# Performance work log

Measured on AMD Instinct MI355X. Metric: run time of the kernel, lower is better.

The kernel has to match this reference:

```python
import jax, jax.numpy as jnp
import numpy as np

B, D, H = 4096, 256, 1024
TRACE_STEPS = 10
T_FINAL = 1.0


def setup_inputs() -> dict:
    key = jax.random.key(0)
    k0, k1, k2 = jax.random.split(key, 3)
    s1 = 1.0 / np.sqrt(D + 1)
    s2 = 1.0 / np.sqrt(H)
    return {
        "x": jax.random.normal(k0, (B, D), dtype=jnp.float32),
        "W1": jax.random.uniform(k1, (D + 1, H), jnp.float32, -s1, s1),
        "b1": jnp.zeros((H,), jnp.float32),
        "W2": jax.random.uniform(k2, (H, D), jnp.float32, -s2, s2),
        "b2": jnp.zeros((D,), jnp.float32),
    }


def _odefun(params, t, z):
    # FFJORD vector field: tanh MLP on [z, t]. z: [B, D] -> [B, D]
    W1, b1, W2, b2 = params
    tcol = jnp.full((z.shape[0], 1), t, dtype=z.dtype)
    h = jnp.tanh(jnp.concatenate([z, tcol], axis=-1) @ W1 + b1)
    return h @ W2 + b2


def _rademacher(key, shape, dtype):
    # randint(0,2)*2-1, matching the torch probe construction
    return jax.random.randint(key, shape, 0, 2).astype(dtype) * 2.0 - 1.0


def _aug_dynamics(params, t, state, e):
    # state: [B, D+1] = [z | logp]; e: [TRACE_STEPS, B, D] Rademacher probes.
    # torch computes etf = grad((f*e).sum(), z) = e^T J, div = (e^T J)*e summed.
    # e^T J e == e . (J e), so forward-mode jvp gives identical math.
    z = state[:, :-1]
    f = lambda zz: _odefun(params, t, zz)

    def probe(ei):
        f_z, Je = jax.jvp(f, (z,), (ei,))
        return f_z, jnp.sum(Je * ei, axis=-1)  # [B]

    f_z, divs = jax.vmap(probe)(e)
    f_z = f_z[0]                       # primal identical across probes
    div_est = jnp.mean(divs, axis=0)   # average of trace_steps estimates
    return jnp.concatenate([f_z, -div_est[:, None]], axis=-1)


def reference(x, W1, b1, W2, b2):
    params = (W1, b1, W2, b2)
    Bx = x.shape[0]
    ekey = jax.random.key(42)
    probes = lambda i: _rademacher(jax.random.fold_in(ekey, i), (TRACE_STEPS, Bx, D), x.dtype)

    # initial augmented state: [z, logp=0]
    y0 = jnp.concatenate([x, jnp.zeros((Bx, 1), x.dtype)], axis=-1)

    # t_grid = [0, T] with 2 points -> fixed-grid rk4 takes ONE RK4 step of size T
    h = T_FINAL
    g = lambda t, y, i: _aug_dynamics(params, t, y, probes(i))
    k1 = g(0.0, y0, 0)
    k2 = g(0.5 * h, y0 + 0.5 * h * k1, 1)
    k3 = g(0.5 * h, y0 + 0.5 * h * k2, 2)
    k4 = g(h, y0 + h * k3, 3)
    y1 = y0 + (h / 6.0) * (k1 + 2.0 * k2 + 2.0 * k3 + k4)

    # module returns the full trajectory `output`: [len(t_grid), B, D+1]
    return jnp.stack([y0, y1], axis=0)
```

## Files before the change

### kernel.cpp

```cpp
#include <hip/hip_runtime.h>
#include <stdint.h>

#define BATCH 4096
#define DIMD  256
#define DIMH  1024
#define NEEL  10485760
#define NSLOT 1310720

typedef __attribute__((ext_vector_type(8))) short short8;
typedef __attribute__((ext_vector_type(4))) float float4v;

struct Keys4 { uint32_t a[4]; uint32_t b[4]; };

__host__ __device__ static inline uint32_t rotl32(uint32_t v, int r) {
#ifdef __HIP_DEVICE_COMPILE__
    return __builtin_amdgcn_alignbit(v, v, 32 - r);
#else
    return (v << r) | (v >> (32 - r));
#endif
}

__host__ __device__ static inline void tf2x32(uint32_t k0, uint32_t k1,
                                              uint32_t c0, uint32_t c1,
                                              uint32_t& o0, uint32_t& o1) {
    uint32_t ks0 = k0, ks1 = k1, ks2 = k0 ^ k1 ^ 0x1BD11BDAu;
    uint32_t x0 = c0 + ks0, x1 = c1 + ks1;
#define TF_R4(a, b, c, d)                                   \
    x0 += x1; x1 = rotl32(x1, a); x1 ^= x0;                 \
    x0 += x1; x1 = rotl32(x1, b); x1 ^= x0;                 \
    x0 += x1; x1 = rotl32(x1, c); x1 ^= x0;                 \
    x0 += x1; x1 = rotl32(x1, d); x1 ^= x0;
    TF_R4(13, 15, 26, 6)  x0 += ks1; x1 += ks2 + 1u;
    TF_R4(17, 29, 16, 24) x0 += ks2; x1 += ks0 + 2u;
    TF_R4(13, 15, 26, 6)  x0 += ks0; x1 += ks1 + 3u;
    TF_R4(17, 29, 16, 24) x0 += ks1; x1 += ks2 + 4u;
    TF_R4(13, 15, 26, 6)  x0 += ks2; x1 += ks0 + 5u;
#undef TF_R4
    o0 = x0; o1 = x1;
}

__device__ static inline short f2bf(float f) {
    uint32_t u = __float_as_uint(f);
    uint32_t r = (u + 0x7FFFu + ((u >> 16) & 1u)) >> 16;
    return (short)r;
}

__device__ static inline void egen_slot(short* __restrict__ EF, uint32_t q,
                                        uint32_t k0, uint32_t k1) {
    const uint32_t lane = q & 63u;
    const uint32_t ks   = (q >> 6) & 7u;
    const uint32_t T    = (q >> 9) & 255u;
    const uint32_t probe = q >> 17;
    const uint32_t b = T * 16u + (lane & 15u);
    const uint32_t d0 = ks * 32u + (lane >> 4) * 8u;
    const uint32_t jbase = (probe * 4096u + b) * 256u + d0;
    short8 val;
#pragma unroll
    for (int jj = 0; jj < 8; ++jj) {
        uint32_t y0, y1;
        tf2x32(k0, k1, 0u, jbase + (uint32_t)jj, y0, y1);
        val[jj] = ((y0 ^ y1) & 1u) ? (short)0x3F80 : (short)0xBF80u;
    }
    *(short8*)&EF[(size_t)q * 8] = val;
}

__global__ __launch_bounds__(256) void k_prep(
    const float* __restrict__ x,  const float* __restrict__ W1,
    const float* __restrict__ W2, short* __restrict__ W1T,
    short* __restrict__ W2B, short* __restrict__ W2T,
    short* __restrict__ zb, float* __restrict__ dv,
    short* __restrict__ E0, uint32_t ek0, uint32_t ek1)
{
    const int idx = blockIdx.x * 256 + threadIdx.x;
    if (idx < 262144) {
        const int n = idx >> 8, d = idx & 255;
        W1T[idx] = f2bf(W1[d * DIMH + n]);
    } else if (idx < 524288) {
        const int i = idx - 262144;
        W2B[i] = f2bf(W2[i]);
    } else if (idx < 786432) {
        const int i = idx - 524288;
        const int d = i >> 10, k = i & 1023;
        W2T[i] = f2bf(W2[k * DIMD + d]);
    } else if (idx < 1835008) {
        const int i = idx - 786432;
        zb[i] = f2bf(x[i]);
    } else if (idx < 1851392) {
        dv[idx - 1835008] = 0.0f;
    } else {
        egen_slot(E0, (uint32_t)(idx - 1851392), ek0, ek1);
    }
}

__global__ __launch_bounds__(256) void k_pre_div(
    const short* __restrict__ Zb, const short* __restrict__ W1T,
    const short* __restrict__ W2B, const float* __restrict__ W1,
    const float* __restrict__ b1, float tval,
    const short* __restrict__ Ecur, short* __restrict__ h_bf,
    float* __restrict__ divacc,
    short* __restrict__ Enext, uint32_t nk0, uint32_t nk1, int do_egen)
{
    __shared__ short8 Es[4096];
    const int t = threadIdx.x;
    const int b0 = blockIdx.x * 64;
    const int nt = blockIdx.y;
    const int wave = t >> 6, lane = t & 63;
    const int col = lane & 15, kq = lane >> 4;
    const int n = nt * 64 + wave * 16 + col;

    short8 bufr[8], bvfr[8];
#pragma unroll
    for (int ks = 0; ks < 8; ++ks) {
        bufr[ks] = *(const short8*)&W1T[n * DIMD + ks * 32 + kq * 8];
        bvfr[ks] = *(const short8*)&W2B[n * DIMD + ks * 32 + kq * 8];
    }

    float sreg[4][4];
    const float add = tval * W1[DIMD * DIMH + n] + b1[n];
#pragma unroll
    for (int ms = 0; ms < 4; ++ms) {
        float4v acc = {0.f, 0.f, 0.f, 0.f};
#pragma unroll
        for (int ks = 0; ks < 8; ++ks) {
            short8 af = *(const short8*)&Zb[(b0 + ms * 16 + col) * DIMD + ks * 32 + kq * 8];
            acc = __builtin_amdgcn_mfma_f32_16x16x32_bf16(af, bufr[ks], acc, 0, 0, 0);
        }
#pragma unroll
        for (int r = 0; r < 4; ++r) {
            float hv = tanhf(acc[r] + add);
            h_bf[(b0 + ms * 16 + kq * 4 + r) * DIMH + n] = f2bf(hv);
            sreg[ms][r] = 1.0f - hv * hv;
        }
    }

    float rowacc[4][4];
#pragma unroll
    for (int a = 0; a < 4; ++a)
#pragma unroll
        for (int r = 0; r < 4; ++r) rowacc[a][r] = 0.0f;

    const uint32_t bflat = (uint32_t)(blockIdx.y * 64 + blockIdx.x);
    const uint32_t qbase = bflat * 256u + (uint32_t)t;

    const int Tb = b0 >> 4;

#pragma unroll 1
    for (int pp = 0; pp < 5; ++pp) {
        if (do_egen) {
            egen_slot(Enext, qbase + (uint32_t)pp * 262144u, nk0, nk1);
        }
        const short8* src0 = (const short8*)Ecur + (size_t)((2 * pp) * 256 + Tb) * 512;
        const short8* src1 = src0 + (size_t)256 * 512;
        __syncthreads();
#pragma unroll
        for (int k = 0; k < 8; ++k)
            Es[t + k * 256] = src0[t + k * 256];
#pragma unroll
        for (int k = 0; k < 8; ++k)
            Es[2048 + t + k * 256] = src1[t + k * 256];
        __syncthreads();

#pragma unroll
        for (int half = 0; half < 2; ++half) {
#pragma unroll
            for (int ms = 0; ms < 4; ++ms) {
                float4v u = {0.f, 0.f, 0.f, 0.f}, v = {0.f, 0.f, 0.f, 0.f};
#pragma unroll
                for (int ks = 0; ks < 8; ++ks) {
                    short8 af = Es[half * 2048 + ((ms * 8 + ks) << 6) + lane];
                    u = __builtin_amdgcn_mfma_f32_16x16x32_bf16(af, bufr[ks], u, 0, 0, 0);
                    v = __builtin_amdgcn_mfma_f32_16x16x32_bf16(af, bvfr[ks], v, 0, 0, 0);
                }
#pragma unroll
                for (int r = 0; r < 4; ++r)
                    rowacc[ms][r] += u[r] * sreg[ms][r] * v[r];
            }
        }
    }

#pragma unroll
    for (int ms = 0; ms < 4; ++ms) {
#pragma unroll
        for (int r = 0; r < 4; ++r) {
            float p = rowacc[ms][r];
            p += __shfl_xor(p, 1, 64);
            p += __shfl_xor(p, 2, 64);
            p += __shfl_xor(p, 4, 64);
            p += __shfl_xor(p, 8, 64);
            rowacc[ms][r] = p;
        }
    }
    if (col == 0) {
#pragma unroll
        for (int ms = 0; ms < 4; ++ms)
#pragma unroll
            for (int r = 0; r < 4; ++r)
                atomicAdd(&divacc[b0 + ms * 16 + kq * 4 + r], rowacc[ms][r] * 0.1f);
    }
}

__global__ __launch_bounds__(256) void k_fz2(
    const short* __restrict__ Hb, const short* __restrict__ W2T,
    const float* __restrict__ b2, const float* __restrict__ x,
    float* __restrict__ rksum, float cw, int first,
    float cnext, int write_zb, short* __restrict__ zb,
    int final_out, const float* __restrict__ dv, float* __restrict__ out)
{
    const int t = threadIdx.x;
    const int wave = t >> 6, lane = t & 63;
    const int col = lane & 15, kq = lane >> 4;
    const int m0 = blockIdx.x * 16;
    const int n0 = wave * 64;
    const int TOT = BATCH * (DIMD + 1);
    const float sixth = 1.0f / 6.0f;

    float4v acc[4];
#pragma unroll
    for (int ns = 0; ns < 4; ++ns) acc[ns] = (float4v){0.f, 0.f, 0.f, 0.f};

    const short* ap = &Hb[(m0 + col) * DIMH + kq * 8];
    short8 a_cur = *(const short8*)ap;
    short8 b_cur[4];
#pragma unroll
    for (int ns = 0; ns < 4; ++ns)
        b_cur[ns] = *(const short8*)&W2T[(n0 + ns * 16 + col) * DIMH + kq * 8];

    for (int ks = 0; ks < 31; ++ks) {
        short8 a_nxt = *(const short8*)&ap[(ks + 1) * 32];
        short8 b_nxt[4];
#pragma unroll
        for (int ns = 0; ns < 4; ++ns)
            b_nxt[ns] = *(const short8*)&W2T[(n0 + ns * 16 + col) * DIMH + (ks + 1) * 32 + kq * 8];
#pragma unroll
        for (int ns = 0; ns < 4; ++ns)
            acc[ns] = __builtin_amdgcn_mfma_f32_16x16x32_bf16(a_cur, b_cur[ns], acc[ns], 0, 0, 0);
        a_cur = a_nxt;
#pragma unroll
        for (int ns = 0; ns < 4; ++ns) b_cur[ns] = b_nxt[ns];
    }
#pragma unroll
    for (int ns = 0; ns < 4; ++ns)
        acc[ns] = __builtin_amdgcn_mfma_f32_16x16x32_bf16(a_cur, b_cur[ns], acc[ns], 0, 0, 0);

#pragma unroll
    for (int ns = 0; ns < 4; ++ns) {
        const int n = n0 + ns * 16 + col;
        const float bias = b2[n];
#pragma unroll
        for (int r = 0; r < 4; ++r) {
            const int m = m0 + kq * 4 + r;
            const int o = m * DIMD + n;
            const float val = acc[ns][r] + bias;
            if (final_out) {
                const float xv = x[o];
                out[m * (DIMD + 1) + n] = xv;
                out[TOT + m * (DIMD + 1) + n] =
                    xv + (rksum[o] + val) * sixth;
            } else {
                const float contrib = cw * val;
                rksum[o] = first ? contrib : (rksum[o] + contrib);
                if (write_zb)
                    zb[o] = f2bf(x[o] + cnext * val);
            }
        }
    }

    if (final_out && wave == 3 && col == 0) {
#pragma unroll
        for (int r = 0; r < 4; ++r) {
            const int m = m0 + kq * 4 + r;
            const float d1 = dv[m];
            const float d2 = dv[BATCH + m];
            const float d3 = dv[2 * BATCH + m];
            const float d4 = dv[3 * BATCH + m];
            out[m * (DIMD + 1) + DIMD] = 0.0f;
            out[TOT + m * (DIMD + 1) + DIMD] =
                -(d1 + 2.0f * d2 + 2.0f * d3 + d4) * sixth;
        }
    }
}

extern "C" void kernel_launch(void* const* d_in, const int* in_sizes, int n_in,
                              void* d_out, int out_size, void* d_ws, size_t ws_size,
                              hipStream_t stream) {
    const float* x  = (const float*)d_in[0];
    const float* W1 = (const float*)d_in[1];
    const float* b1 = (const float*)d_in[2];
    const float* W2 = (const float*)d_in[3];
    const float* b2 = (const float*)d_in[4];
    float* out = (float*)d_out;

    char* ws = (char*)d_ws;
    short* hb    = (short*)(ws);
    float* rksum = (float*)(ws + 8388608);
    short* zb    = (short*)(ws + 12582912);
    short* w1t   = (short*)(ws + 14680064);
    short* w2b   = (short*)(ws + 15204352);
    short* w2t   = (short*)(ws + 15728640);
    float* dv    = (float*)(ws + 16252928);
    short* e0    = (short*)(ws + 16318464);
    short* e1    = (short*)(ws + 37289984);

    Keys4 keys;
    for (uint32_t i = 0; i < 4; ++i) {
        uint32_t f0, f1, g0, g1;
        tf2x32(0u, 42u, 0u, i, f0, f1);
        tf2x32(f0, f1, 0u, 1u, g0, g1);
        keys.a[i] = g0;
        keys.b[i] = g1;
    }

    k_prep<<<12352, 256, 0, stream>>>(x, W1, W2, w1t, w2b, w2t, zb, dv,
                                      e0, keys.a[0], keys.b[0]);

    const float tvals[4] = {0.0f, 0.5f, 0.5f, 1.0f};
    const float cnext[4] = {0.5f, 0.5f, 1.0f, 0.0f};
    const float cw[4]    = {1.0f, 2.0f, 2.0f, 1.0f};
    for (int s = 0; s < 4; ++s) {
        const int last = (s == 3);
        short* ecur = (s & 1) ? e1 : e0;
        short* enxt = (s & 1) ? e0 : e1;
        k_pre_div<<<dim3(64, 16), 256, 0, stream>>>(
            zb, w1t, w2b, W1, b1, tvals[s], ecur,
            hb, dv + (size_t)s * BATCH,
            enxt, last ? 0u : keys.a[s + 1], last ? 0u : keys.b[s + 1],
            last ? 0 : 1);
        k_fz2<<<256, 256, 0, stream>>>(hb, w2t, b2, x, rksum,
                                       cw[s], (s == 0) ? 1 : 0,
                                       cnext[s], (s < 3) ? 1 : 0, zb,
                                       last ? 1 : 0, dv, out);
    }
}
```

Baseline: 482.6 us.

## Double-buffer probe tiles with async global-to-LDS loads and split output GEMM grid

```diff
diff --git a/kernel.cpp b/kernel.cpp
--- a/kernel.cpp
+++ b/kernel.cpp
@@ -43,6 +43,12 @@
     uint32_t u = __float_as_uint(f);
     uint32_t r = (u + 0x7FFFu + ((u >> 16) & 1u)) >> 16;
     return (short)r;
+}
+
+__device__ static inline void async_cp16(const void* gsrc, void* ldst) {
+    typedef __attribute__((address_space(1))) const unsigned int GU;
+    typedef __attribute__((address_space(3))) unsigned int LU;
+    __builtin_amdgcn_global_load_lds((GU*)gsrc, (LU*)ldst, 16, 0, 0);
 }
 
 __device__ static inline void egen_slot(short* __restrict__ EF, uint32_t q,
@@ -100,13 +106,29 @@
     float* __restrict__ divacc,
     short* __restrict__ Enext, uint32_t nk0, uint32_t nk1, int do_egen)
 {
-    __shared__ short8 Es[4096];
+    __shared__ short8 Es[2][2048];
     const int t = threadIdx.x;
     const int b0 = blockIdx.x * 64;
     const int nt = blockIdx.y;
     const int wave = t >> 6, lane = t & 63;
     const int col = lane & 15, kq = lane >> 4;
     const int n = nt * 64 + wave * 16 + col;
+    const int Tb = b0 >> 4;
+
+    const short8* Ebase = (const short8*)Ecur;
+    auto stage = [&](int p) {
+        const short8* src = Ebase + (size_t)(p * 256 + Tb) * 512 + wave * 64;
+        short8* dst = &Es[p & 1][wave * 64];
+#pragma unroll
+        for (int k = 0; k < 8; ++k)
+            async_cp16(src + k * 256 + lane, dst + k * 256);
+    };
+    stage(0);
+    stage(1);
+
+    const uint32_t bflat = (uint32_t)(blockIdx.y * 64 + blockIdx.x);
+    const uint32_t qbase = bflat * 256u + (uint32_t)t;
+    if (do_egen) egen_slot(Enext, qbase, nk0, nk1);
 
     short8 bufr[8], bvfr[8];
 #pragma unroll
@@ -139,43 +161,32 @@
 #pragma unroll
         for (int r = 0; r < 4; ++r) rowacc[a][r] = 0.0f;
 
-    const uint32_t bflat = (uint32_t)(blockIdx.y * 64 + blockIdx.x);
-    const uint32_t qbase = bflat * 256u + (uint32_t)t;
-
-    const int Tb = b0 >> 4;
-
 #pragma unroll 1
-    for (int pp = 0; pp < 5; ++pp) {
-        if (do_egen) {
-            egen_slot(Enext, qbase + (uint32_t)pp * 262144u, nk0, nk1);
-        }
-        const short8* src0 = (const short8*)Ecur + (size_t)((2 * pp) * 256 + Tb) * 512;
-        const short8* src1 = src0 + (size_t)256 * 512;
-        __syncthreads();
-#pragma unroll
-        for (int k = 0; k < 8; ++k)
-            Es[t + k * 256] = src0[t + k * 256];
-#pragma unroll
-        for (int k = 0; k < 8; ++k)
-            Es[2048 + t + k * 256] = src1[t + k * 256];
-        __syncthreads();
-
-#pragma unroll
-        for (int half = 0; half < 2; ++half) {
-#pragma unroll
-            for (int ms = 0; ms < 4; ++ms) {
-                float4v u = {0.f, 0.f, 0.f, 0.f}, v = {0.f, 0.f, 0.f, 0.f};
-#pragma unroll
-                for (int ks = 0; ks < 8; ++ks) {
-                    short8 af = Es[half * 2048 + ((ms * 8 + ks) << 6) + lane];
-                    u = __builtin_amdgcn_mfma_f32_16x16x32_bf16(af, bufr[ks], u, 0, 0, 0);
-                    v = __builtin_amdgcn_mfma_f32_16x16x32_bf16(af, bvfr[ks], v, 0, 0, 0);
-                }
-#pragma unroll
-                for (int r = 0; r < 4; ++r)
-                    rowacc[ms][r] += u[r] * sreg[ms][r] * v[r];
+    for (int pp = 0; pp < 10; ++pp) {
+        if (pp < 9) { asm volatile("s_waitcnt vmcnt(8)" ::: "memory"); }
+        else        { asm volatile("s_waitcnt vmcnt(0)" ::: "memory"); }
+        __builtin_amdgcn_s_barrier();
+
+        const short8* buf = (const short8*)Es[pp & 1];
+#pragma unroll
+        for (int ms = 0; ms < 4; ++ms) {
+            float4v u = {0.f, 0.f, 0.f, 0.f}, v = {0.f, 0.f, 0.f, 0.f};
+#pragma unroll
+            for (int ks = 0; ks < 8; ++ks) {
+                short8 af = buf[ms * 512 + ks * 64 + lane];
+                u = __builtin_amdgcn_mfma_f32_16x16x32_bf16(af, bufr[ks], u, 0, 0, 0);
+                v = __builtin_amdgcn_mfma_f32_16x16x32_bf16(af, bvfr[ks], v, 0, 0, 0);
             }
-        }
+#pragma unroll
+            for (int r = 0; r < 4; ++r)
+                rowacc[ms][r] += u[r] * sreg[ms][r] * v[r];
+        }
+
+        asm volatile("" ::: "memory");
+        __builtin_amdgcn_s_barrier();
+        if (pp < 8) stage(pp + 2);
+        if (do_egen && (pp & 1) == 0 && pp <= 6)
+            egen_slot(Enext, qbase + (uint32_t)(1 + (pp >> 1)) * 262144u, nk0, nk1);
     }
 
 #pragma unroll
@@ -210,51 +221,38 @@
     const int wave = t >> 6, lane = t & 63;
     const int col = lane & 15, kq = lane >> 4;
     const int m0 = blockIdx.x * 16;
-    const int n0 = wave * 64;
+    const int n0 = blockIdx.y * 64 + wave * 16;
     const int TOT = BATCH * (DIMD + 1);
     const float sixth = 1.0f / 6.0f;
 
-    float4v acc[4];
-#pragma unroll
-    for (int ns = 0; ns < 4; ++ns) acc[ns] = (float4v){0.f, 0.f, 0.f, 0.f};
+    float4v acc = {0.f, 0.f, 0.f, 0.f};
 
     const short* ap = &Hb[(m0 + col) * DIMH + kq * 8];
+    const short* bp = &W2T[(n0 + col) * DIMH + kq * 8];
     short8 a_cur = *(const short8*)ap;
-    short8 b_cur[4];
-#pragma unroll
-    for (int ns = 0; ns < 4; ++ns)
-        b_cur[ns] = *(const short8*)&W2T[(n0 + ns * 16 + col) * DIMH + kq * 8];
+    short8 b_cur = *(const short8*)bp;
 
     for (int ks = 0; ks < 31; ++ks) {
         short8 a_nxt = *(const short8*)&ap[(ks + 1) * 32];
-        short8 b_nxt[4];
-#pragma unroll
-        for (int ns = 0; ns < 4; ++ns)
-            b_nxt[ns] = *(const short8*)&W2T[(n0 + ns * 16 + col) * DIMH + (ks + 1) * 32 + kq * 8];
-#pragma unroll
-        for (int ns = 0; ns < 4; ++ns)
-            acc[ns] = __builtin_amdgcn_mfma_f32_16x16x32_bf16(a_cur, b_cur[ns], acc[ns], 0, 0, 0);
+        short8 b_nxt = *(const short8*)&bp[(ks + 1) * 32];
+        acc = __builtin_amdgcn_mfma_f32_16x16x32_bf16(a_cur, b_cur, acc, 0, 0, 0);
         a_cur = a_nxt;
-#pragma unroll
-        for (int ns = 0; ns < 4; ++ns) b_cur[ns] = b_nxt[ns];
-    }
-#pragma unroll
-    for (int ns = 0; ns < 4; ++ns)
-        acc[ns] = __builtin_amdgcn_mfma_f32_16x16x32_bf16(a_cur, b_cur[ns], acc[ns], 0, 0, 0);
-
-#pragma unroll
-    for (int ns = 0; ns < 4; ++ns) {
-        const int n = n0 + ns * 16 + col;
-        const float bias = b2[n];
+        b_cur = b_nxt;
+    }
+    acc = __builtin_amdgcn_mfma_f32_16x16x32_bf16(a_cur, b_cur, acc, 0, 0, 0);
+
+    {
+        const int nn = n0 + col;
+        const float bias = b2[nn];
 #pragma unroll
         for (int r = 0; r < 4; ++r) {
             const int m = m0 + kq * 4 + r;
-            const int o = m * DIMD + n;
-            const float val = acc[ns][r] + bias;
+            const int o = m * DIMD + nn;
+            const float val = acc[r] + bias;
             if (final_out) {
                 const float xv = x[o];
-                out[m * (DIMD + 1) + n] = xv;
-                out[TOT + m * (DIMD + 1) + n] =
+                out[m * (DIMD + 1) + nn] = xv;
+                out[TOT + m * (DIMD + 1) + nn] =
                     xv + (rksum[o] + val) * sixth;
             } else {
                 const float contrib = cw * val;
@@ -265,7 +263,7 @@
         }
     }
 
-    if (final_out && wave == 3 && col == 0) {
+    if (final_out && blockIdx.y == 0 && wave == 0 && col == 0) {
 #pragma unroll
         for (int r = 0; r < 4; ++r) {
             const int m = m0 + kq * 4 + r;
@@ -325,9 +323,9 @@
             hb, dv + (size_t)s * BATCH,
             enxt, last ? 0u : keys.a[s + 1], last ? 0u : keys.b[s + 1],
             last ? 0 : 1);
-        k_fz2<<<256, 256, 0, stream>>>(hb, w2t, b2, x, rksum,
-                                       cw[s], (s == 0) ? 1 : 0,
-                                       cnext[s], (s < 3) ? 1 : 0, zb,
-                                       last ? 1 : 0, dv, out);
-    }
-}
+        k_fz2<<<dim3(256, 4), 256, 0, stream>>>(hb, w2t, b2, x, rksum,
+                                                cw[s], (s == 0) ? 1 : 0,
+                                                cnext[s], (s < 3) ? 1 : 0, zb,
+                                                last ? 1 : 0, dv, out);
+    }
+}
```

After: 490.2 us. No clear change (+1.6%).
